# Kernel optimization log

Hardware: AMD Instinct MI355X
Metric: run time of the kernel (lower is better)

Reference implementation:

```python
import jax, jax.numpy as jnp
import numpy as np

N_NODES = 20000
N_EDGES = 320000
N_GRAPHS = 32
IN_CH = 5
HID = 64
HEADS = 4
DH = HID // HEADS  # 16
LAYERS = 8
EPS = 1e-5
SLOPE = 0.2


def setup_inputs() -> dict:
    key = jax.random.key(0)
    ks = jax.random.split(key, 32)
    inp = {}
    inp['x1'] = jax.random.normal(ks[0], (N_NODES, IN_CH), dtype=jnp.float32)
    inp['x2'] = jax.random.normal(ks[1], (N_NODES, IN_CH), dtype=jnp.float32)
    inp['edge_index1'] = jax.random.randint(ks[2], (2, N_EDGES), 0, N_NODES, dtype=jnp.int32)
    inp['edge_index2'] = jax.random.randint(ks[3], (2, N_EDGES), 0, N_NODES, dtype=jnp.int32)
    inp['batch1'] = jnp.sort(jax.random.randint(ks[4], (N_NODES,), 0, N_GRAPHS, dtype=jnp.int32))
    inp['batch2'] = jnp.sort(jax.random.randint(ks[5], (N_NODES,), 0, N_GRAPHS, dtype=jnp.int32))
    # node_lin
    inp['Wn'] = jax.random.normal(ks[6], (IN_CH, HID), dtype=jnp.float32) / np.sqrt(IN_CH)
    inp['bnode'] = jnp.zeros((HID,), dtype=jnp.float32)
    # GATv2 layers (stacked over LAYERS)
    s = 1.0 / np.sqrt(HID)
    inp['Wl'] = jax.random.normal(ks[7], (LAYERS, HID, HID), dtype=jnp.float32) * s
    inp['bl'] = jnp.zeros((LAYERS, HID), dtype=jnp.float32)
    inp['Wr'] = jax.random.normal(ks[8], (LAYERS, HID, HID), dtype=jnp.float32) * s
    inp['br'] = jnp.zeros((LAYERS, HID), dtype=jnp.float32)
    inp['att'] = jax.random.normal(ks[9], (LAYERS, HEADS, DH), dtype=jnp.float32) / np.sqrt(DH)
    inp['cbias'] = jnp.zeros((LAYERS, HID), dtype=jnp.float32)
    # batch norms
    inp['gamma'] = jnp.ones((LAYERS, HID), dtype=jnp.float32)
    inp['beta'] = jnp.zeros((LAYERS, HID), dtype=jnp.float32)
    # fc head
    inp['f1w'] = jax.random.normal(ks[10], (2 * HID, 256), dtype=jnp.float32) / np.sqrt(2 * HID)
    inp['f1b'] = jnp.zeros((256,), dtype=jnp.float32)
    inp['f2w'] = jax.random.normal(ks[11], (256, 128), dtype=jnp.float32) / np.sqrt(256)
    inp['f2b'] = jnp.zeros((128,), dtype=jnp.float32)
    inp['f3w'] = jax.random.normal(ks[12], (128, 1), dtype=jnp.float32) / np.sqrt(128)
    inp['f3b'] = jnp.zeros((1,), dtype=jnp.float32)
    return inp


def _gatv2_layer(x, src, dst, Wl, bl, Wr, br, att, bias):
    # x: [N, HID]; src/dst: [E'] (self loops included)
    N = x.shape[0]
    xl = (x @ Wl + bl).reshape(N, HEADS, DH)  # source transform
    xr = (x @ Wr + br).reshape(N, HEADS, DH)  # target transform
    e = jax.nn.leaky_relu(xl[src] + xr[dst], SLOPE)          # [E, H, DH]
    score = jnp.einsum('ehd,hd->eh', e, att)                  # [E, H]
    smax = jax.ops.segment_max(score, dst, num_segments=N)    # [N, H]
    ex = jnp.exp(score - smax[dst])
    denom = jax.ops.segment_sum(ex, dst, num_segments=N)
    alpha = ex / denom[dst]                                   # [E, H]
    msg = alpha[:, :, None] * xl[src]                         # [E, H, DH]
    out = jax.ops.segment_sum(msg, dst, num_segments=N)       # [N, H, DH]
    return out.reshape(N, HID) + bias


def _forward_once(x, edge_index, batch, Wn, bnode, Wl, bl, Wr, br, att, cbias, gamma, beta):
    N = x.shape[0]
    loop = jnp.arange(N, dtype=edge_index.dtype)
    src = jnp.concatenate([edge_index[0], loop])  # add_self_loops=True
    dst = jnp.concatenate([edge_index[1], loop])
    h = x @ Wn + bnode
    for l in range(LAYERS):
        g = _gatv2_layer(h, src, dst, Wl[l], bl[l], Wr[l], br[l], att[l], cbias[l])
        mu = g.mean(axis=0)
        var = g.var(axis=0)
        g = (g - mu) / jnp.sqrt(var + EPS) * gamma[l] + beta[l]
        h = h + jax.nn.elu(g)
    # global_mean_pool
    sums = jax.ops.segment_sum(h, batch, num_segments=N_GRAPHS)
    cnt = jax.ops.segment_sum(jnp.ones((N,), dtype=h.dtype), batch, num_segments=N_GRAPHS)
    return sums / jnp.maximum(cnt, 1.0)[:, None]


def reference(x1, edge_index1, batch1, x2, edge_index2, batch2, Wn, bnode, Wl, bl, Wr, br, att, cbias, gamma, beta, f1w, f1b, f2w, f2b, f3w, f3b):
    o1 = _forward_once(x1, edge_index1, batch1, Wn, bnode, Wl, bl, Wr, br, att, cbias, gamma, beta)
    o2 = _forward_once(x2, edge_index2, batch2, Wn, bnode, Wl, bl, Wr, br, att, cbias, gamma, beta)
    c = jnp.concatenate([o1, o2], axis=1)           # [G, 128]
    h = jax.nn.relu(c @ f1w + f1b)                   # dropout = identity (eval)
    h = jax.nn.relu(h @ f2w + f2b)
    return h @ f3w + f3b                             # [G, 1]
```

## Files before the change

### kernel.cpp

```cpp
#include <hip/hip_runtime.h>
#include <hip/hip_bf16.h>
#include <hip/hip_fp16.h>

#define N_NODES 20000
#define HID 64
#define EPS 1e-5f

struct GP {
    const int* ei;
    const int* batch;
    const float* x;
    int* deg;
    int* cursor;
    int* csr;
    float* h;
    __half* xlh0;
    __half* xlh1;
    float* xr;
    float* gb;
    float* stats;
    float* osum;
};


__global__ void k_csr_init(GP a, GP b, int n, int two) {
    int t = blockIdx.x * blockDim.x + threadIdx.x;
    if (t < n) {
        a.deg[t] = 1;
        if (two) b.deg[t] = 1;
    }
}

__global__ void k_count(GP a, GP b, int Ea, int Eb, int two) {
    int t = blockIdx.x * blockDim.x + threadIdx.x;
    if (t < Ea) atomicAdd(&a.deg[a.ei[Ea + t]], 1);
    if (two && t < Eb) atomicAdd(&b.deg[b.ei[Eb + t]], 1);
}

#define SCAN_T 1024
#define SCAN_C 20
__global__ __launch_bounds__(1024) void k_scan(GP a, GP b, int n, int totA, int totB) {
    GP g = blockIdx.x ? b : a;
    int total = blockIdx.x ? totB : totA;
    __shared__ int sd[SCAN_T];
    int t = threadIdx.x;
    int base = t * SCAN_C;
    int loc[SCAN_C];
    int s = 0;
#pragma unroll
    for (int i = 0; i < SCAN_C; ++i) {
        int idx = base + i;
        loc[i] = (idx < n) ? g.deg[idx] : 0;
        s += loc[i];
    }
    sd[t] = s;
    __syncthreads();
    for (int off = 1; off < SCAN_T; off <<= 1) {
        int v = (t >= off) ? sd[t - off] : 0;
        __syncthreads();
        sd[t] += v;
        __syncthreads();
    }
    int run = sd[t] - s;
#pragma unroll
    for (int i = 0; i < SCAN_C; ++i) {
        int idx = base + i;
        if (idx < n) { g.deg[idx] = run; g.cursor[idx] = run; run += loc[i]; }
    }
    if (t == 0) g.deg[n] = total;
}

__global__ void k_scatter(GP a, GP b, int Ea, int Eb, int n, int two) {
    int t = blockIdx.x * blockDim.x + threadIdx.x;
    if (t < Ea) {
        int s = a.ei[t], d = a.ei[Ea + t];
        a.csr[atomicAdd(&a.cursor[d], 1)] = s * 64;
    } else if (t < Ea + n) {
        int nn = t - Ea;
        a.csr[atomicAdd(&a.cursor[nn], 1)] = nn * 64;
    }
    if (two) {
        if (t < Eb) {
            int s = b.ei[t], d = b.ei[Eb + t];
            b.csr[atomicAdd(&b.cursor[d], 1)] = s * 64;
        } else if (t < Eb + n) {
            int nn = t - Eb;
            b.csr[atomicAdd(&b.cursor[nn], 1)] = nn * 64;
        }
    }
}


__global__ void k_nodelin(GP a, GP b, int nPer, const float* __restrict__ Wn,
                          const float* __restrict__ bn, int n) {
    int bid = blockIdx.x;
    GP g = a;
    if (bid >= nPer) { g = b; bid -= nPer; }
    int idx = bid * 256 + threadIdx.x;
    if (idx >= n * HID) return;
    int node = idx >> 6, c = idx & 63;
    float acc = bn[c];
#pragma unroll
    for (int k = 0; k < 5; ++k) acc += g.x[node * 5 + k] * Wn[k * HID + c];
    g.h[idx] = acc;
}


__global__ __launch_bounds__(256) void k_lin2(GP ga, GP gbp, int nPer, int n,
        const float* __restrict__ Wl, const float* __restrict__ bl,
        const float* __restrict__ Wr, const float* __restrict__ br,
        const float* __restrict__ gamma, const float* __restrict__ beta, int layer) {
    __shared__ float wls[4096], wrs[4096];
    __shared__ float hs[2048];
    int bid = blockIdx.x;
    GP g = ga;
    if (bid >= nPer) { g = gbp; bid -= nPer; }
    {
        const float4* wl4 = (const float4*)Wl;
        const float4* wr4 = (const float4*)Wr;
        float4* l4 = (float4*)wls;
        float4* r4 = (float4*)wrs;
        for (int i = threadIdx.x; i < 1024; i += 256) { l4[i] = wl4[i]; r4[i] = wr4[i]; }
    }
    int c = threadIdx.x & 63;
    int wid = threadIdx.x >> 6;
    float blv = bl[c], brv = br[c];
    float mu = 0.f, inv = 1.f, gam = 1.f, bet = 0.f;
    if (layer > 0) {
        const float* st = g.stats + (layer - 1) * 128;
        float invn = 1.0f / (float)n;
        mu = st[c] * invn;
        float var = st[64 + c] * invn - mu * mu;
        inv = rsqrtf(fmaxf(var, 0.f) + EPS);
        gam = gamma[c]; bet = beta[c];
    }
    __syncthreads();
    float* hw = &hs[wid * 512];
    const float4* hw4 = (const float4*)hw;
    __half* xbase = (c < 32) ? g.xlh0 : g.xlh1;
    int cc = c & 31;
    for (int base = bid * 32; base < n; base += nPer * 32) {
        int nb = base + wid * 8;
        size_t off0 = (size_t)nb * 64 + c;
        float hv[8];
        if (layer > 0) {
#pragma unroll
            for (int j = 0; j < 8; ++j) {
                float gv = g.gb[off0 + j * 64];
                float ov = g.h[off0 + j * 64];
                float v = (gv - mu) * inv * gam + bet;
                v = v > 0.f ? v : expm1f(v);
                hv[j] = ov + v;
                g.h[off0 + j * 64] = hv[j];
            }
        } else {
#pragma unroll
            for (int j = 0; j < 8; ++j) hv[j] = g.h[off0 + j * 64];
        }
#pragma unroll
        for (int j = 0; j < 8; ++j) hw[j * 64 + c] = hv[j];
        float accl[8], accr[8];
#pragma unroll
        for (int j = 0; j < 8; ++j) { accl[j] = blv; accr[j] = brv; }
        for (int k4 = 0; k4 < 16; ++k4) {
            float4 hq[8];
#pragma unroll
            for (int j = 0; j < 8; ++j) hq[j] = hw4[j * 16 + k4];
#pragma unroll
            for (int kk = 0; kk < 4; ++kk) {
                float wl = wls[(k4 * 4 + kk) * 64 + c];
                float wr = wrs[(k4 * 4 + kk) * 64 + c];
#pragma unroll
                for (int j = 0; j < 8; ++j) {
                    float hx = (&hq[j].x)[kk];
                    accl[j] = fmaf(hx, wl, accl[j]);
                    accr[j] = fmaf(hx, wr, accr[j]);
                }
            }
        }
#pragma unroll
        for (int j = 0; j < 8; ++j) {
            xbase[(size_t)(nb + j) * 32 + cc] = __float2half(accl[j]);
            g.xr[off0 + j * 64] = accr[j];
        }
    }
}


__device__ __forceinline__ float red16(float p) {
    p += __int_as_float(__builtin_amdgcn_update_dpp(0, __float_as_int(p), 0xB1, 0xF, 0xF, true));
    p += __int_as_float(__builtin_amdgcn_update_dpp(0, __float_as_int(p), 0x4E, 0xF, 0xF, true));
    p += __int_as_float(__builtin_amdgcn_update_dpp(0, __float_as_int(p), 0x141, 0xF, 0xF, true));
    p += __int_as_float(__builtin_amdgcn_update_dpp(0, __float_as_int(p), 0x140, 0xF, 0xF, true));
    return p;
}

__global__ __launch_bounds__(1024) void k_attn(GP ga, GP gbp, int nPer,
        const float* __restrict__ att, const float* __restrict__ cbias, int layer, int n) {
    int bid = blockIdx.x;
    GP g = (bid & 1) ? gbp : ga;
    bid >>= 1;
    int lane = threadIdx.x & 63;
    int wid = threadIdx.x >> 6;
    int h = lane >> 5;
    int cl = lane & 31;
    int gw = bid * 16 + wid;
    int nw = nPer * 16;
    const int* __restrict__ rowptr = g.deg;
    const int* __restrict__ csr = g.csr;
    const float* __restrict__ xr = g.xr;
    float* __restrict__ gbuf = g.gb;
    float* st = g.stats + layer * 128;
    __shared__ float sred[1024];
    for (int pass = 0; pass < 2; ++pass) {
        const char* xlb = (const char*)(pass ? g.xlh1 : g.xlh0) + (size_t)cl * 2;
        float attv = att[pass * 32 + cl] * 1.44269504f;
        float attv2 = attv * 0.2f;
        float cb = cbias[pass * 32 + cl];
        float bsum = 0.f, bsq = 0.f;
        for (int node = gw; node < n; node += nw) {
            int start = rowptr[node], end = rowptr[node + 1];
            float xrv = xr[(size_t)node * 64 + pass * 32 + cl];
            float xself = __half2float(*(const __half*)(xlb + (size_t)node * 64));
            float ts = xself + xrv;
            float sself = red16(ts * (ts > 0.f ? attv : attv2));
            float lsum = 0.f, acc = 0.f;
            int idx = start;
            for (; idx + 8 <= end; idx += 8) {
                int off[4];
                float xv[4];
#pragma unroll
                for (int j = 0; j < 4; ++j) off[j] = csr[idx + 2 * j + h];
#pragma unroll
                for (int j = 0; j < 4; ++j) xv[j] = __half2float(*(const __half*)(xlb + off[j]));
#pragma unroll
                for (int j = 0; j < 4; ++j) {
                    float t = xv[j] + xrv;
                    float p = red16(t * (t > 0.f ? attv : attv2));
                    float w = exp2f(fminf(p - sself, 110.f));
                    lsum += w;
                    acc = fmaf(w, xv[j], acc);
                }
            }
            for (; idx < end; idx += 2) {
                int e = idx + h;
                bool valid = e < end;
                int ec = valid ? e : end - 1;
                int off = csr[ec];
                float xv = __half2float(*(const __half*)(xlb + off));
                float t = xv + xrv;
                float p = red16(t * (t > 0.f ? attv : attv2));
                float w = exp2f(fminf(p - sself, 110.f));
                w = valid ? w : 0.f;
                lsum += w;
                acc = fmaf(w, xv, acc);
            }
            lsum += __shfl_xor(lsum, 32);
            acc += __shfl_xor(acc, 32);
            float outv = acc / lsum + cb;
            if (h == 0) {
                gbuf[(size_t)node * 64 + pass * 32 + cl] = outv;
                bsum += outv; bsq += outv * outv;
            }
        }
        sred[threadIdx.x] = (h == 0) ? bsum : 0.f;
        __syncthreads();
        if (threadIdx.x < 32) {
            float t = 0.f;
#pragma unroll
            for (int w = 0; w < 16; ++w) t += sred[w * 64 + threadIdx.x];
            atomicAdd(&st[pass * 32 + threadIdx.x], t);
        }
        __syncthreads();
        sred[threadIdx.x] = (h == 0) ? bsq : 0.f;
        __syncthreads();
        if (threadIdx.x < 32) {
            float t = 0.f;
#pragma unroll
            for (int w = 0; w < 16; ++w) t += sred[w * 64 + threadIdx.x];
            atomicAdd(&st[64 + pass * 32 + threadIdx.x], t);
        }
        __syncthreads();
    }
}


__global__ __launch_bounds__(256) void k_pool(GP ga, GP gbp, int nPer,
        const float* __restrict__ gamma, const float* __restrict__ beta, int n) {
    int bid = blockIdx.x;
    GP g = ga;
    if (bid >= nPer) { g = gbp; bid -= nPer; }
    int lane = threadIdx.x & 63, w = threadIdx.x >> 6;
    const float* st = g.stats + 7 * 128;
    float invn = 1.f / (float)n;
    float mu = st[lane] * invn;
    float var = st[64 + lane] * invn - mu * mu;
    float inv = rsqrtf(fmaxf(var, 0.f) + EPS);
    float gam = gamma[lane], bet = beta[lane];
    int chunk = (n + nPer - 1) / nPer;
    int s = bid * chunk;
    int e = min(s + chunk, n);
    float acc = 0.f;
    int cur = -1;
    for (int node = s + w; node < e; node += 4) {
        int bg = g.batch[node];
        size_t off = (size_t)node * 64 + lane;
        float gv = g.gb[off];
        float hv = g.h[off];
        float v = (gv - mu) * inv * gam + bet;
        float hn = hv + (v > 0.f ? v : expm1f(v));
        if (bg != cur) {
            if (cur >= 0) atomicAdd(&g.osum[cur * 64 + lane], acc);
            acc = 0.f; cur = bg;
        }
        acc += hn;
    }
    if (cur >= 0) atomicAdd(&g.osum[cur * 64 + lane], acc);
}


__device__ __forceinline__ int lb(const int* __restrict__ b, int n, int v) {
    int lo = 0, hi = n;
    while (lo < hi) { int mid = (lo + hi) >> 1; if (b[mid] < v) lo = mid + 1; else hi = mid; }
    return lo;
}

__global__ __launch_bounds__(256) void k_fc(const float* __restrict__ o1, const float* __restrict__ o2,
                                            const int* __restrict__ b1, const int* __restrict__ b2,
                                            const float* __restrict__ f1w, const float* __restrict__ f1b,
                                            const float* __restrict__ f2w, const float* __restrict__ f2b,
                                            const float* __restrict__ f3w, const float* __restrict__ f3b,
                                            float* __restrict__ out, int n) {
    int gid = blockIdx.x, t = threadIdx.x;
    __shared__ float cin[128];
    __shared__ float h1[256];
    __shared__ float red[128];
    __shared__ int cnts[2];
    if (t == 0) cnts[0] = lb(b1, n, gid + 1) - lb(b1, n, gid);
    if (t == 1) cnts[1] = lb(b2, n, gid + 1) - lb(b2, n, gid);
    __syncthreads();
    if (t < 64) {
        float c1 = (float)(cnts[0] > 0 ? cnts[0] : 1);
        float c2 = (float)(cnts[1] > 0 ? cnts[1] : 1);
        cin[t] = o1[gid * 64 + t] / c1;
        cin[64 + t] = o2[gid * 64 + t] / c2;
    }
    __syncthreads();
    float a = f1b[t];
#pragma unroll 8
    for (int k = 0; k < 128; ++k) a += cin[k] * f1w[k * 256 + t];
    h1[t] = fmaxf(a, 0.f);
    __syncthreads();
    if (t < 128) {
        float a2 = f2b[t];
#pragma unroll 8
        for (int k = 0; k < 256; ++k) a2 += h1[k] * f2w[k * 128 + t];
        red[t] = fmaxf(a2, 0.f) * f3w[t];
    }
    __syncthreads();
    for (int off = 64; off > 0; off >>= 1) {
        if (t < off) red[t] += red[t + off];
        __syncthreads();
    }
    if (t == 0) out[gid] = red[0] + f3b[0];
}


extern "C" void kernel_launch(void* const* d_in, const int* in_sizes, int n_in,
                              void* d_out, int out_size, void* d_ws, size_t ws_size,
                              hipStream_t stream) {
    const float* x1 = (const float*)d_in[0];
    const float* x2 = (const float*)d_in[1];
    const int* ei1 = (const int*)d_in[2];
    const int* ei2 = (const int*)d_in[3];
    const int* b1 = (const int*)d_in[4];
    const int* b2 = (const int*)d_in[5];
    const float* Wn = (const float*)d_in[6];
    const float* bnode = (const float*)d_in[7];
    const float* Wl = (const float*)d_in[8];
    const float* bl = (const float*)d_in[9];
    const float* Wr = (const float*)d_in[10];
    const float* br = (const float*)d_in[11];
    const float* att = (const float*)d_in[12];
    const float* cbias = (const float*)d_in[13];
    const float* gamma = (const float*)d_in[14];
    const float* beta = (const float*)d_in[15];
    const float* f1w = (const float*)d_in[16];
    const float* f1b = (const float*)d_in[17];
    const float* f2w = (const float*)d_in[18];
    const float* f2b = (const float*)d_in[19];
    const float* f3w = (const float*)d_in[20];
    const float* f3b = (const float*)d_in[21];
    float* out = (float*)d_out;

    const int N = N_NODES;
    const int EA = in_sizes[2] / 2;
    const int EB = in_sizes[3] / 2;
    const size_t INT_PG = 20096 + 20096 + 340096;
    const size_t BIG = (size_t)N * 64;
    const size_t SMALL = 2 * 1024 + 2 * 2048;
    const size_t dualBytes = 2 * INT_PG * 4 + (8 * BIG + SMALL) * 4;
    const int dual = (ws_size >= dualBytes) ? 1 : 0;

    int* ibase = (int*)d_ws;
    int* iA = ibase;
    int* iB = dual ? ibase + INT_PG : ibase;
    float* fbase = (float*)(ibase + (size_t)(dual ? 2 : 1) * INT_PG);
    float* hA = fbase;
    float* xlA = hA + BIG;
    float* xrA = xlA + BIG;
    float* gbA = xrA + BIG;
    float* hB = dual ? gbA + BIG : hA;
    float* xlB = dual ? hB + BIG : xlA;
    float* xrB = dual ? xlB + BIG : xrA;
    float* gbB = dual ? xrB + BIG : gbA;
    float* small = dual ? gbB + BIG : gbA + BIG;
    float* statsA = small;
    float* statsB = small + 1024;
    float* osumA = small + 2048;
    float* osumB = small + 4096;

    GP A, B;
    A.ei = ei1; A.batch = b1; A.x = x1;
    A.deg = iA; A.cursor = iA + 20096; A.csr = iA + 40192;
    A.h = hA; A.xlh0 = (__half*)xlA; A.xlh1 = (__half*)xlA + (size_t)N * 32;
    A.xr = xrA; A.gb = gbA; A.stats = statsA; A.osum = osumA;
    B.ei = ei2; B.batch = b2; B.x = x2;
    B.deg = iB; B.cursor = iB + 20096; B.csr = iB + 40192;
    B.h = hB; B.xlh0 = (__half*)xlB; B.xlh1 = (__half*)xlB + (size_t)N * 32;
    B.xr = xrB; B.gb = gbB; B.stats = statsB; B.osum = osumB;

    hipMemsetAsync(small, 0, SMALL * sizeof(float), stream);

    const int LIN2_NB = 320;
    const int ATT_NB = 256;
    const int POOL_NB = 250;

    if (dual) {
        int Emax = EA > EB ? EA : EB;
        k_csr_init<<<(N + 255) / 256, 256, 0, stream>>>(A, B, N, 1);
        k_count<<<(Emax + 255) / 256, 256, 0, stream>>>(A, B, EA, EB, 1);
        k_scan<<<2, 1024, 0, stream>>>(A, B, N, EA + N, EB + N);
        k_scatter<<<(Emax + N + 255) / 256, 256, 0, stream>>>(A, B, EA, EB, N, 1);
        k_nodelin<<<2 * ((N * 64) / 256), 256, 0, stream>>>(A, B, (N * 64) / 256, Wn, bnode, N);
        for (int l = 0; l < 8; ++l) {
            const float* gm = l ? gamma + (l - 1) * 64 : gamma;
            const float* bt = l ? beta + (l - 1) * 64 : beta;
            k_lin2<<<2 * LIN2_NB, 256, 0, stream>>>(A, B, LIN2_NB, N, Wl + l * 4096, bl + l * 64,
                                                    Wr + l * 4096, br + l * 64, gm, bt, l);
            k_attn<<<2 * ATT_NB, 1024, 0, stream>>>(A, B, ATT_NB, att + l * 64, cbias + l * 64, l, N);
        }
        k_pool<<<2 * POOL_NB, 256, 0, stream>>>(A, B, POOL_NB, gamma + 7 * 64, beta + 7 * 64, N);
    } else {
        for (int gi = 0; gi < 2; ++gi) {
            GP G = gi ? B : A;
            int E = gi ? EB : EA;
            k_csr_init<<<(N + 255) / 256, 256, 0, stream>>>(G, G, N, 0);
            k_count<<<(E + 255) / 256, 256, 0, stream>>>(G, G, E, E, 0);
            k_scan<<<1, 1024, 0, stream>>>(G, G, N, E + N, E + N);
            k_scatter<<<(E + N + 255) / 256, 256, 0, stream>>>(G, G, E, E, N, 0);
            k_nodelin<<<(N * 64) / 256, 256, 0, stream>>>(G, G, (N * 64) / 256, Wn, bnode, N);
            for (int l = 0; l < 8; ++l) {
                const float* gm = l ? gamma + (l - 1) * 64 : gamma;
                const float* bt = l ? beta + (l - 1) * 64 : beta;
                k_lin2<<<LIN2_NB, 256, 0, stream>>>(G, G, LIN2_NB, N, Wl + l * 4096, bl + l * 64,
                                                    Wr + l * 4096, br + l * 64, gm, bt, l);
                k_attn<<<2 * ATT_NB, 1024, 0, stream>>>(G, G, ATT_NB, att + l * 64, cbias + l * 64, l, N);
            }
            k_pool<<<POOL_NB, 256, 0, stream>>>(G, G, POOL_NB, gamma + 7 * 64, beta + 7 * 64, N);
        }
    }
    k_fc<<<32, 256, 0, stream>>>(osumA, osumB, b1, b2, f1w, f1b, f2w, f2b, f3w, f3b, out, N);
}
```

Measured before the change: 778.4 us.

## Process both head-halves in one attention pass with packed fp16 pairs

The attention kernel now handles all 64 channels in a single pass: each lane owns two adjacent channels loaded as a packed half2, so each 8-lane group covers one head and the reduction drops to three DPP steps. xl and xr are stored interleaved as full 64-channel fp16 rows instead of split halves, with xr also moved to fp16. The leaky-relu is computed in packed half arithmetic. This halves the CSR index traffic and the per-edge reduction count and shrinks xr reads, at the cost of extra fp16 rounding in xr and in the pre-activation sum.

```diff
diff --git a/kernel.cpp b/kernel.cpp
--- a/kernel.cpp
+++ b/kernel.cpp
@@ -5,6 +5,8 @@
 #define N_NODES 20000
 #define HID 64
 #define EPS 1e-5f
+
+typedef _Float16 h2 __attribute__((ext_vector_type(2)));
 
 struct GP {
     const int* ei;
@@ -14,9 +16,8 @@
     int* cursor;
     int* csr;
     float* h;
-    __half* xlh0;
-    __half* xlh1;
-    float* xr;
+    __half* xlh;
+    __half* xrh;
     float* gb;
     float* stats;
     float* osum;
@@ -74,18 +75,18 @@
     int t = blockIdx.x * blockDim.x + threadIdx.x;
     if (t < Ea) {
         int s = a.ei[t], d = a.ei[Ea + t];
-        a.csr[atomicAdd(&a.cursor[d], 1)] = s * 64;
+        a.csr[atomicAdd(&a.cursor[d], 1)] = s * 128;
     } else if (t < Ea + n) {
         int nn = t - Ea;
-        a.csr[atomicAdd(&a.cursor[nn], 1)] = nn * 64;
+        a.csr[atomicAdd(&a.cursor[nn], 1)] = nn * 128;
     }
     if (two) {
         if (t < Eb) {
             int s = b.ei[t], d = b.ei[Eb + t];
-            b.csr[atomicAdd(&b.cursor[d], 1)] = s * 64;
+            b.csr[atomicAdd(&b.cursor[d], 1)] = s * 128;
         } else if (t < Eb + n) {
             int nn = t - Eb;
-            b.csr[atomicAdd(&b.cursor[nn], 1)] = nn * 64;
+            b.csr[atomicAdd(&b.cursor[nn], 1)] = nn * 128;
         }
     }
 }
@@ -137,8 +138,6 @@
     __syncthreads();
     float* hw = &hs[wid * 512];
     const float4* hw4 = (const float4*)hw;
-    __half* xbase = (c < 32) ? g.xlh0 : g.xlh1;
-    int cc = c & 31;
     for (int base = bid * 32; base < n; base += nPer * 32) {
         int nb = base + wid * 8;
         size_t off0 = (size_t)nb * 64 + c;
@@ -180,18 +179,17 @@
         }
 #pragma unroll
         for (int j = 0; j < 8; ++j) {
-            xbase[(size_t)(nb + j) * 32 + cc] = __float2half(accl[j]);
-            g.xr[off0 + j * 64] = accr[j];
-        }
-    }
-}
-
-
-__device__ __forceinline__ float red16(float p) {
+            g.xlh[off0 + j * 64] = __float2half(accl[j]);
+            g.xrh[off0 + j * 64] = __float2half(accr[j]);
+        }
+    }
+}
+
+
+__device__ __forceinline__ float red8(float p) {
     p += __int_as_float(__builtin_amdgcn_update_dpp(0, __float_as_int(p), 0xB1, 0xF, 0xF, true));
     p += __int_as_float(__builtin_amdgcn_update_dpp(0, __float_as_int(p), 0x4E, 0xF, 0xF, true));
     p += __int_as_float(__builtin_amdgcn_update_dpp(0, __float_as_int(p), 0x141, 0xF, 0xF, true));
-    p += __int_as_float(__builtin_amdgcn_update_dpp(0, __float_as_int(p), 0x140, 0xF, 0xF, true));
     return p;
 }
 
@@ -202,85 +200,102 @@
     bid >>= 1;
     int lane = threadIdx.x & 63;
     int wid = threadIdx.x >> 6;
-    int h = lane >> 5;
+    int hh = lane >> 5;
     int cl = lane & 31;
     int gw = bid * 16 + wid;
     int nw = nPer * 16;
+    const float LOG2E = 1.44269504f;
+    float a0 = att[2 * cl] * LOG2E;
+    float a1 = att[2 * cl + 1] * LOG2E;
+    float cb0 = cbias[2 * cl], cb1 = cbias[2 * cl + 1];
+    const h2 slope = {(_Float16)0.2f, (_Float16)0.2f};
     const int* __restrict__ rowptr = g.deg;
     const int* __restrict__ csr = g.csr;
-    const float* __restrict__ xr = g.xr;
+    const char* xlb = (const char*)g.xlh + (size_t)cl * 4;
+    const char* xrb = (const char*)g.xrh + (size_t)cl * 4;
     float* __restrict__ gbuf = g.gb;
     float* st = g.stats + layer * 128;
-    __shared__ float sred[1024];
-    for (int pass = 0; pass < 2; ++pass) {
-        const char* xlb = (const char*)(pass ? g.xlh1 : g.xlh0) + (size_t)cl * 2;
-        float attv = att[pass * 32 + cl] * 1.44269504f;
-        float attv2 = attv * 0.2f;
-        float cb = cbias[pass * 32 + cl];
-        float bsum = 0.f, bsq = 0.f;
-        for (int node = gw; node < n; node += nw) {
-            int start = rowptr[node], end = rowptr[node + 1];
-            float xrv = xr[(size_t)node * 64 + pass * 32 + cl];
-            float xself = __half2float(*(const __half*)(xlb + (size_t)node * 64));
-            float ts = xself + xrv;
-            float sself = red16(ts * (ts > 0.f ? attv : attv2));
-            float lsum = 0.f, acc = 0.f;
-            int idx = start;
-            for (; idx + 8 <= end; idx += 8) {
-                int off[4];
-                float xv[4];
-#pragma unroll
-                for (int j = 0; j < 4; ++j) off[j] = csr[idx + 2 * j + h];
-#pragma unroll
-                for (int j = 0; j < 4; ++j) xv[j] = __half2float(*(const __half*)(xlb + off[j]));
-#pragma unroll
-                for (int j = 0; j < 4; ++j) {
-                    float t = xv[j] + xrv;
-                    float p = red16(t * (t > 0.f ? attv : attv2));
-                    float w = exp2f(fminf(p - sself, 110.f));
-                    lsum += w;
-                    acc = fmaf(w, xv[j], acc);
-                }
+    float bs0 = 0.f, bs1 = 0.f, bq0 = 0.f, bq1 = 0.f;
+    for (int node = gw; node < n; node += nw) {
+        int start = rowptr[node], end = rowptr[node + 1];
+        h2 xrv = *(const h2*)(xrb + (size_t)node * 128);
+        float sself;
+        {
+            h2 xs = *(const h2*)(xlb + (size_t)node * 128);
+            h2 t = xs + xrv;
+            h2 lk = __builtin_elementwise_max(t, t * slope);
+            float sp = fmaf((float)lk.x, a0, (float)lk.y * a1);
+            sself = red8(sp);
+        }
+        float lsum = 0.f, acc0 = 0.f, acc1 = 0.f;
+        int idx = start;
+        for (; idx + 8 <= end; idx += 8) {
+            int off[4];
+            h2 xv[4];
+#pragma unroll
+            for (int j = 0; j < 4; ++j) off[j] = csr[idx + 2 * j + hh];
+#pragma unroll
+            for (int j = 0; j < 4; ++j) xv[j] = *(const h2*)(xlb + off[j]);
+#pragma unroll
+            for (int j = 0; j < 4; ++j) {
+                h2 t = xv[j] + xrv;
+                h2 lk = __builtin_elementwise_max(t, t * slope);
+                float sp = fmaf((float)lk.x, a0, (float)lk.y * a1);
+                float w = exp2f(fminf(red8(sp) - sself, 110.f));
+                lsum += w;
+                acc0 = fmaf(w, (float)xv[j].x, acc0);
+                acc1 = fmaf(w, (float)xv[j].y, acc1);
             }
-            for (; idx < end; idx += 2) {
-                int e = idx + h;
-                bool valid = e < end;
-                int ec = valid ? e : end - 1;
-                int off = csr[ec];
-                float xv = __half2float(*(const __half*)(xlb + off));
-                float t = xv + xrv;
-                float p = red16(t * (t > 0.f ? attv : attv2));
-                float w = exp2f(fminf(p - sself, 110.f));
-                w = valid ? w : 0.f;
-                lsum += w;
-                acc = fmaf(w, xv, acc);
-            }
-            lsum += __shfl_xor(lsum, 32);
-            acc += __shfl_xor(acc, 32);
-            float outv = acc / lsum + cb;
-            if (h == 0) {
-                gbuf[(size_t)node * 64 + pass * 32 + cl] = outv;
-                bsum += outv; bsq += outv * outv;
-            }
-        }
-        sred[threadIdx.x] = (h == 0) ? bsum : 0.f;
-        __syncthreads();
-        if (threadIdx.x < 32) {
-            float t = 0.f;
-#pragma unroll
-            for (int w = 0; w < 16; ++w) t += sred[w * 64 + threadIdx.x];
-            atomicAdd(&st[pass * 32 + threadIdx.x], t);
-        }
-        __syncthreads();
-        sred[threadIdx.x] = (h == 0) ? bsq : 0.f;
-        __syncthreads();
-        if (threadIdx.x < 32) {
-            float t = 0.f;
-#pragma unroll
-            for (int w = 0; w < 16; ++w) t += sred[w * 64 + threadIdx.x];
-            atomicAdd(&st[64 + pass * 32 + threadIdx.x], t);
-        }
-        __syncthreads();
+        }
+        for (; idx < end; idx += 2) {
+            int e = idx + hh;
+            bool valid = e < end;
+            int off = csr[valid ? e : end - 1];
+            h2 xv = *(const h2*)(xlb + off);
+            h2 t = xv + xrv;
+            h2 lk = __builtin_elementwise_max(t, t * slope);
+            float sp = fmaf((float)lk.x, a0, (float)lk.y * a1);
+            float w = exp2f(fminf(red8(sp) - sself, 110.f));
+            w = valid ? w : 0.f;
+            lsum += w;
+            acc0 = fmaf(w, (float)xv.x, acc0);
+            acc1 = fmaf(w, (float)xv.y, acc1);
+        }
+        lsum += __shfl_xor(lsum, 32);
+        acc0 += __shfl_xor(acc0, 32);
+        acc1 += __shfl_xor(acc1, 32);
+        if (hh == 0) {
+            float invl = 1.0f / lsum;
+            float o0 = acc0 * invl + cb0;
+            float o1 = acc1 * invl + cb1;
+            float2 o = {o0, o1};
+            *(float2*)(gbuf + (size_t)node * 64 + 2 * cl) = o;
+            bs0 += o0; bs1 += o1;
+            bq0 += o0 * o0; bq1 += o1 * o1;
+        }
+    }
+    __shared__ float2 sred[1024];
+    float2 z = {0.f, 0.f};
+    float2 v1 = {bs0, bs1};
+    sred[threadIdx.x] = (hh == 0) ? v1 : z;
+    __syncthreads();
+    if (threadIdx.x < 32) {
+        float t0 = 0.f, t1 = 0.f;
+#pragma unroll
+        for (int w = 0; w < 16; ++w) { float2 s = sred[w * 64 + threadIdx.x]; t0 += s.x; t1 += s.y; }
+        atomicAdd(&st[2 * threadIdx.x], t0);
+        atomicAdd(&st[2 * threadIdx.x + 1], t1);
+    }
+    __syncthreads();
+    float2 v2 = {bq0, bq1};
+    sred[threadIdx.x] = (hh == 0) ? v2 : z;
+    __syncthreads();
+    if (threadIdx.x < 32) {
+        float t0 = 0.f, t1 = 0.f;
+#pragma unroll
+        for (int w = 0; w < 16; ++w) { float2 s = sred[w * 64 + threadIdx.x]; t0 += s.x; t1 += s.y; }
+        atomicAdd(&st[64 + 2 * threadIdx.x], t0);
+        atomicAdd(&st[64 + 2 * threadIdx.x + 1], t1);
     }
 }
 
@@ -423,12 +438,12 @@
     GP A, B;
     A.ei = ei1; A.batch = b1; A.x = x1;
     A.deg = iA; A.cursor = iA + 20096; A.csr = iA + 40192;
-    A.h = hA; A.xlh0 = (__half*)xlA; A.xlh1 = (__half*)xlA + (size_t)N * 32;
-    A.xr = xrA; A.gb = gbA; A.stats = statsA; A.osum = osumA;
+    A.h = hA; A.xlh = (__half*)xlA; A.xrh = (__half*)xrA;
+    A.gb = gbA; A.stats = statsA; A.osum = osumA;
     B.ei = ei2; B.batch = b2; B.x = x2;
     B.deg = iB; B.cursor = iB + 20096; B.csr = iB + 40192;
-    B.h = hB; B.xlh0 = (__half*)xlB; B.xlh1 = (__half*)xlB + (size_t)N * 32;
-    B.xr = xrB; B.gb = gbB; B.stats = statsB; B.osum = osumB;
+    B.h = hB; B.xlh = (__half*)xlB; B.xrh = (__half*)xrB;
+    B.gb = gbB; B.stats = statsB; B.osum = osumB;
 
     hipMemsetAsync(small, 0, SMALL * sizeof(float), stream);
 
```

Result: faster. 660.5 us (-15.1%).
